# Kernel tuning notes

Measured on AMD Instinct MI355X. Metric: run time of the kernel, lower is better.

The kernel has to match this reference:

```python
import jax, jax.numpy as jnp
import numpy as np

N = 50000      # num nodes
HID = 64       # hidden_dim
N2V = 64       # node2vec dim
E = 800000     # num edges
EP = 100000    # prediction edges
L = 2          # num_layers
EPS = 1e-5     # BatchNorm eps


def setup_inputs() -> dict:
    key = jax.random.key(0)
    ks = jax.random.split(key, 8)
    edge_index = jax.random.randint(ks[0], (2, E), 0, N)
    pred_edge = jax.random.randint(ks[1], (EP, 2), 0, N)
    id_emb = jax.random.normal(ks[2], (N, HID), jnp.float32) * 0.1      # learnable ID embedding
    n2v_emb = jax.random.normal(ks[3], (N, N2V), jnp.float32) * 0.1     # frozen node2vec embedding
    proj_w = jax.random.normal(ks[4], (HID + N2V, HID), jnp.float32) / np.sqrt(HID + N2V)
    proj_b = jnp.zeros((HID,), jnp.float32)
    conv_w = jax.random.normal(ks[5], (L, HID, HID), jnp.float32) / np.sqrt(HID)
    conv_b = jnp.zeros((L, HID), jnp.float32)
    bn_gamma = jnp.ones((L, HID), jnp.float32)
    bn_beta = jnp.zeros((L, HID), jnp.float32)
    return {"edge_index": edge_index, "pred_edge": pred_edge, "id_emb": id_emb,
            "n2v_emb": n2v_emb, "proj_w": proj_w, "proj_b": proj_b,
            "conv_w": conv_w, "conv_b": conv_b, "bn_gamma": bn_gamma, "bn_beta": bn_beta}


def reference(edge_index, pred_edge, id_emb, n2v_emb, proj_w, proj_b, conv_w, conv_b, bn_gamma, bn_beta):
    # input projection of concatenated embeddings: [N, HID+N2V] @ [HID+N2V, HID]
    x = jnp.concatenate([id_emb, n2v_emb], axis=1) @ proj_w + proj_b

    # GCN normalization with self-loops: norm_e = d^-1/2[src] * d^-1/2[dst]
    loops = jnp.arange(N, dtype=edge_index.dtype)
    row = jnp.concatenate([edge_index[0], loops])   # source nodes
    col = jnp.concatenate([edge_index[1], loops])   # destination nodes
    deg = jax.ops.segment_sum(jnp.ones(row.shape, x.dtype), col, num_segments=N)
    dis = jnp.where(deg > 0, jax.lax.rsqrt(deg), 0.0)
    norm = dis[row] * dis[col]                      # [E+N]

    for l in range(L):
        h = x @ conv_w[l]                                                    # [N, HID]
        agg = jax.ops.segment_sum(norm[:, None] * h[row], col, num_segments=N) + conv_b[l]
        # BatchNorm1d (training-mode batch stats over nodes)
        mu = agg.mean(axis=0)
        var = agg.var(axis=0)
        xn = (agg - mu) * jax.lax.rsqrt(var + EPS) * bn_gamma[l] + bn_beta[l]
        x = x + jax.nn.relu(xn)                                              # residual (shapes match)

    # dot-product link decoder
    z = x
    return (z[pred_edge[:, 0]] * z[pred_edge[:, 1]]).sum(axis=1)
```

## Files before the change

### kernel.cpp

```cpp
#include <hip/hip_runtime.h>

#define NN 50000
#define HID 64
#define NE 800000
#define NP 100000
#define BN_EPS 1e-5f
#define NB1 196
#define MAXDEG 96

static inline size_t alignup(size_t x) { return (x + 255) & ~(size_t)255; }

__device__ __forceinline__ void f4fma(float a, const float4& w, float4& c) {
    c.x += a * w.x; c.y += a * w.y; c.z += a * w.z; c.w += a * w.w;
}
__device__ __forceinline__ void f4add(const float4& a, float4& c) {
    c.x += a.x; c.y += a.y; c.z += a.z; c.w += a.w;
}
__device__ __forceinline__ unsigned bfpack(float a, float b) {
    unsigned ua = __float_as_uint(a), ub = __float_as_uint(b);
    ua = (ua + 0x7fffu + ((ua >> 16) & 1u)) >> 16;
    ub = (ub + 0x7fffu + ((ub >> 16) & 1u)) >> 16;
    return ua | (ub << 16);
}
__device__ __forceinline__ float4 bf2f4(uint2 u) {
    float4 r;
    r.x = __uint_as_float(u.x << 16);
    r.y = __uint_as_float(u.x & 0xffff0000u);
    r.z = __uint_as_float(u.y << 16);
    r.w = __uint_as_float(u.y & 0xffff0000u);
    return r;
}


__global__ __launch_bounds__(256) void k_zero(int* __restrict__ cnt, float* __restrict__ sums) {
    int i = blockIdx.x * blockDim.x + threadIdx.x;
    if (i < NN) cnt[i] = 0;
    if (i < 256) sums[i] = 0.f;
}


__global__ __launch_bounds__(256) void k_countfill(const int* __restrict__ row,
                                                   const int* __restrict__ col,
                                                   int* __restrict__ cnt,
                                                   unsigned short* __restrict__ csr) {
    int e = blockIdx.x * blockDim.x + threadIdx.x;
    if (e >= NE) return;
    int d = col[e];
    int r = atomicAdd(&cnt[d], 1);
    csr[d * MAXDEG + r] = (unsigned short)row[e];
}


__global__ __launch_bounds__(256) void k_proj(const float* __restrict__ id_emb,
                                              const float* __restrict__ n2v,
                                              const float* __restrict__ W,
                                              const float* __restrict__ b,
                                              const int* __restrict__ cnt,
                                              float* __restrict__ x,
                                              unsigned short* __restrict__ xh) {
    __shared__ unsigned short Wlh[128 * 64];
    __shared__ unsigned short Al[32 * 132];
    int tid = threadIdx.x;
    int node0 = blockIdx.x * 32;
    const float2* W2f = (const float2*)W;
#pragma unroll
    for (int it = 0; it < 16; ++it) {
        int i = it * 256 + tid;
        float2 w = W2f[i];
        *(unsigned*)&Wlh[2 * i] = bfpack(w.x, w.y);
    }
    const float2* id2 = (const float2*)id_emb;
    const float2* nv2 = (const float2*)n2v;
#pragma unroll
    for (int it = 0; it < 8; ++it) {
        int i = it * 256 + tid;
        int r = i >> 6, kp = i & 63;
        int n = node0 + r;
        float2 v = make_float2(0.f, 0.f);
        if (n < NN) v = (kp < 32) ? id2[n * 32 + kp] : nv2[n * 32 + (kp - 32)];
        *(unsigned*)&Al[r * 132 + 2 * kp] = bfpack(v.x, v.y);
    }
    __syncthreads();
    int sub = tid >> 4, q = tid & 15;
    const uint2* W2 = (const uint2*)Wlh;
    float4* x4 = (float4*)x;
    uint2* xh2 = (uint2*)xh;
    float4 bb = ((const float4*)b)[q];
    float4 c0 = bb, c1 = bb;
#pragma unroll 4
    for (int k4 = 0; k4 < 32; ++k4) {
        float4 w0 = bf2f4(W2[(k4 * 4 + 0) * 16 + q]);
        float4 w1 = bf2f4(W2[(k4 * 4 + 1) * 16 + q]);
        float4 w2 = bf2f4(W2[(k4 * 4 + 2) * 16 + q]);
        float4 w3 = bf2f4(W2[(k4 * 4 + 3) * 16 + q]);
        float4 a0 = bf2f4(*(const uint2*)&Al[(sub * 2 + 0) * 132 + k4 * 4]);
        float4 a1 = bf2f4(*(const uint2*)&Al[(sub * 2 + 1) * 132 + k4 * 4]);
        f4fma(a0.x, w0, c0); f4fma(a0.y, w1, c0); f4fma(a0.z, w2, c0); f4fma(a0.w, w3, c0);
        f4fma(a1.x, w0, c1); f4fma(a1.y, w1, c1); f4fma(a1.z, w2, c1); f4fma(a1.w, w3, c1);
    }
    int n0 = node0 + sub * 2;
    if (n0 + 0 < NN) { float d = rsqrtf((float)(cnt[n0+0] + 1)); x4[(n0+0)*16+q] = c0;
        xh2[(n0+0)*16+q] = make_uint2(bfpack(c0.x*d,c0.y*d), bfpack(c0.z*d,c0.w*d)); }
    if (n0 + 1 < NN) { float d = rsqrtf((float)(cnt[n0+1] + 1)); x4[(n0+1)*16+q] = c1;
        xh2[(n0+1)*16+q] = make_uint2(bfpack(c1.x*d,c1.y*d), bfpack(c1.z*d,c1.w*d)); }
}


__global__ __launch_bounds__(256) void k_gather(const int* __restrict__ cnt,
                                                const unsigned short* __restrict__ csr,
                                                const unsigned short* __restrict__ xh,
                                                unsigned short* __restrict__ th) {
    int gw = (blockIdx.x * blockDim.x + threadIdx.x) >> 6;
    int lane = threadIdx.x & 63;
    int sub = lane >> 4, q = lane & 15;
    int node = gw * 4 + sub;
    if (node >= NN) return;
    const uint2* xh2 = (const uint2*)xh;
    float4 acc = make_float4(0.f, 0.f, 0.f, 0.f);
    const unsigned short* cs = csr + node * MAXDEG;
    int c = cnt[node];
    int jj = 0;
    for (; jj + 7 < c; jj += 8) {
        uint4 s8 = *(const uint4*)(cs + jj);
        int s0 = s8.x & 0xffff, s1 = s8.x >> 16;
        int s2 = s8.y & 0xffff, s3 = s8.y >> 16;
        int s4 = s8.z & 0xffff, s5 = s8.z >> 16;
        int s6 = s8.w & 0xffff, s7 = s8.w >> 16;
        uint2 u0 = xh2[s0 * 16 + q];
        uint2 u1 = xh2[s1 * 16 + q];
        uint2 u2 = xh2[s2 * 16 + q];
        uint2 u3 = xh2[s3 * 16 + q];
        uint2 u4 = xh2[s4 * 16 + q];
        uint2 u5 = xh2[s5 * 16 + q];
        uint2 u6 = xh2[s6 * 16 + q];
        uint2 u7 = xh2[s7 * 16 + q];
        f4add(bf2f4(u0), acc); f4add(bf2f4(u1), acc);
        f4add(bf2f4(u2), acc); f4add(bf2f4(u3), acc);
        f4add(bf2f4(u4), acc); f4add(bf2f4(u5), acc);
        f4add(bf2f4(u6), acc); f4add(bf2f4(u7), acc);
    }
    for (; jj < c; ++jj) {
        uint2 u0 = xh2[cs[jj] * 16 + q];
        f4add(bf2f4(u0), acc);
    }
    f4add(bf2f4(xh2[node * 16 + q]), acc);
    float di = rsqrtf((float)(c + 1));
    acc.x *= di; acc.y *= di; acc.z *= di; acc.w *= di;
    ((uint2*)th)[node * 16 + q] = make_uint2(bfpack(acc.x, acc.y), bfpack(acc.z, acc.w));
}


__global__ __launch_bounds__(256) void k_gemm_stats(const unsigned short* __restrict__ th,
                                                    const float* __restrict__ W,
                                                    unsigned short* __restrict__ agg,
                                                    float* __restrict__ sums) {
    __shared__ float Wl[64 * 64];
    __shared__ float ls0[16][64];
    __shared__ float ls1[16][64];
    int tid = threadIdx.x;
    for (int i = tid; i < 64 * 64; i += 256) Wl[i] = W[i];
    __syncthreads();
    int sub = tid >> 4, q = tid & 15;
    const uint2* t2 = (const uint2*)th;
    const float4* W4 = (const float4*)Wl;
    uint2* agg2 = (uint2*)agg;
    float4 s1 = make_float4(0.f, 0.f, 0.f, 0.f), s2 = s1;
#pragma unroll
    for (int gg = 0; gg < 2; ++gg) {
        int g = blockIdx.x * 2 + gg;
        int n0 = g * 64 + sub * 4;
        int r0 = min(n0 + 0, NN - 1), r1 = min(n0 + 1, NN - 1);
        int r2 = min(n0 + 2, NN - 1), r3 = min(n0 + 3, NN - 1);
        float4 c0 = make_float4(0.f,0.f,0.f,0.f), c1 = c0, c2 = c0, c3 = c0;
#pragma unroll 4
        for (int k4 = 0; k4 < 16; ++k4) {
            float4 a0 = bf2f4(t2[r0 * 16 + k4]);
            float4 a1 = bf2f4(t2[r1 * 16 + k4]);
            float4 a2 = bf2f4(t2[r2 * 16 + k4]);
            float4 a3 = bf2f4(t2[r3 * 16 + k4]);
            float4 w0 = W4[(k4 * 4 + 0) * 16 + q];
            float4 w1 = W4[(k4 * 4 + 1) * 16 + q];
            float4 w2 = W4[(k4 * 4 + 2) * 16 + q];
            float4 w3 = W4[(k4 * 4 + 3) * 16 + q];
            f4fma(a0.x, w0, c0); f4fma(a0.y, w1, c0); f4fma(a0.z, w2, c0); f4fma(a0.w, w3, c0);
            f4fma(a1.x, w0, c1); f4fma(a1.y, w1, c1); f4fma(a1.z, w2, c1); f4fma(a1.w, w3, c1);
            f4fma(a2.x, w0, c2); f4fma(a2.y, w1, c2); f4fma(a2.z, w2, c2); f4fma(a2.w, w3, c2);
            f4fma(a3.x, w0, c3); f4fma(a3.y, w1, c3); f4fma(a3.z, w2, c3); f4fma(a3.w, w3, c3);
        }
        if (n0 + 0 < NN) { agg2[(n0 + 0) * 16 + q] = make_uint2(bfpack(c0.x, c0.y), bfpack(c0.z, c0.w));
            s1.x += c0.x; s1.y += c0.y; s1.z += c0.z; s1.w += c0.w;
            s2.x += c0.x*c0.x; s2.y += c0.y*c0.y; s2.z += c0.z*c0.z; s2.w += c0.w*c0.w; }
        if (n0 + 1 < NN) { agg2[(n0 + 1) * 16 + q] = make_uint2(bfpack(c1.x, c1.y), bfpack(c1.z, c1.w));
            s1.x += c1.x; s1.y += c1.y; s1.z += c1.z; s1.w += c1.w;
            s2.x += c1.x*c1.x; s2.y += c1.y*c1.y; s2.z += c1.z*c1.z; s2.w += c1.w*c1.w; }
        if (n0 + 2 < NN) { agg2[(n0 + 2) * 16 + q] = make_uint2(bfpack(c2.x, c2.y), bfpack(c2.z, c2.w));
            s1.x += c2.x; s1.y += c2.y; s1.z += c2.z; s1.w += c2.w;
            s2.x += c2.x*c2.x; s2.y += c2.y*c2.y; s2.z += c2.z*c2.z; s2.w += c2.w*c2.w; }
        if (n0 + 3 < NN) { agg2[(n0 + 3) * 16 + q] = make_uint2(bfpack(c3.x, c3.y), bfpack(c3.z, c3.w));
            s1.x += c3.x; s1.y += c3.y; s1.z += c3.z; s1.w += c3.w;
            s2.x += c3.x*c3.x; s2.y += c3.y*c3.y; s2.z += c3.z*c3.z; s2.w += c3.w*c3.w; }
    }
    ls0[sub][q * 4 + 0] = s1.x; ls0[sub][q * 4 + 1] = s1.y;
    ls0[sub][q * 4 + 2] = s1.z; ls0[sub][q * 4 + 3] = s1.w;
    ls1[sub][q * 4 + 0] = s2.x; ls1[sub][q * 4 + 1] = s2.y;
    ls1[sub][q * 4 + 2] = s2.z; ls1[sub][q * 4 + 3] = s2.w;
    __syncthreads();
    if (tid < 64) {
        float a = 0.f;
#pragma unroll
        for (int r = 0; r < 16; ++r) a += ls0[r][tid];
        atomicAdd(&sums[tid], a);
    } else if (tid < 128) {
        int c = tid - 64;
        float a = 0.f;
#pragma unroll
        for (int r = 0; r < 16; ++r) a += ls1[r][c];
        atomicAdd(&sums[64 + c], a);
    }
}


__global__ __launch_bounds__(256) void k_bnupdate(const unsigned short* __restrict__ agg,
                                                  const float* __restrict__ sums,
                                                  const float* __restrict__ gamma,
                                                  const float* __restrict__ beta,
                                                  const int* __restrict__ cnt,
                                                  int prescale,
                                                  float* __restrict__ x,
                                                  unsigned short* __restrict__ xh) {
    int i = blockIdx.x * blockDim.x + threadIdx.x;
    if (i >= NN * 16) return;
    int f4 = i & 15;
    const float invn = 1.0f / (float)NN;
    float4 sm = ((const float4*)sums)[f4];
    float4 sq = ((const float4*)(sums + 64))[f4];
    float4 g = ((const float4*)gamma)[f4];
    float4 be = ((const float4*)beta)[f4];
    float4 a = bf2f4(((const uint2*)agg)[i]);
    float4 xv = ((const float4*)x)[i];
    float mu, var, rstd, xn;
    mu = sm.x * invn; var = sq.x * invn - mu * mu; rstd = rsqrtf(var + BN_EPS);
    xn = (a.x - mu) * rstd * g.x + be.x; xv.x += fmaxf(xn, 0.f);
    mu = sm.y * invn; var = sq.y * invn - mu * mu; rstd = rsqrtf(var + BN_EPS);
    xn = (a.y - mu) * rstd * g.y + be.y; xv.y += fmaxf(xn, 0.f);
    mu = sm.z * invn; var = sq.z * invn - mu * mu; rstd = rsqrtf(var + BN_EPS);
    xn = (a.z - mu) * rstd * g.z + be.z; xv.z += fmaxf(xn, 0.f);
    mu = sm.w * invn; var = sq.w * invn - mu * mu; rstd = rsqrtf(var + BN_EPS);
    xn = (a.w - mu) * rstd * g.w + be.w; xv.w += fmaxf(xn, 0.f);
    if (prescale) {
        ((float4*)x)[i] = xv;
        float d = rsqrtf((float)(cnt[i >> 4] + 1));
        ((uint2*)xh)[i] = make_uint2(bfpack(xv.x * d, xv.y * d), bfpack(xv.z * d, xv.w * d));
    } else {
        ((uint2*)xh)[i] = make_uint2(bfpack(xv.x, xv.y), bfpack(xv.z, xv.w));
    }
}


__global__ __launch_bounds__(256) void k_decode(const int* __restrict__ pred,
                                                const unsigned short* __restrict__ zh,
                                                float* __restrict__ out) {
    int gw = (blockIdx.x * blockDim.x + threadIdx.x) >> 6;
    int lane = threadIdx.x & 63;
    int sub = lane >> 4, q = lane & 15;
    int p = gw * 4 + sub;
    if (p >= NP) return;
    const uint2* z2 = (const uint2*)zh;
    int a = pred[2 * p], b = pred[2 * p + 1];
    float4 va = bf2f4(z2[a * 16 + q]);
    float4 vb = bf2f4(z2[b * 16 + q]);
    float v = va.x * vb.x + va.y * vb.y + va.z * vb.z + va.w * vb.w;
    v += __shfl_xor(v, 1);
    v += __shfl_xor(v, 2);
    v += __shfl_xor(v, 4);
    v += __shfl_xor(v, 8);
    if (q == 0) out[p] = v;
}

extern "C" void kernel_launch(void* const* d_in, const int* in_sizes, int n_in,
                              void* d_out, int out_size, void* d_ws, size_t ws_size,
                              hipStream_t stream) {
    const int* edge_index = (const int*)d_in[0];
    const int* pred       = (const int*)d_in[1];
    const float* id_emb   = (const float*)d_in[2];
    const float* n2v      = (const float*)d_in[3];
    const float* proj_w   = (const float*)d_in[4];
    const float* proj_b   = (const float*)d_in[5];
    const float* conv_w   = (const float*)d_in[6];
    const float* gamma    = (const float*)d_in[8];
    const float* beta     = (const float*)d_in[9];
    float* out = (float*)d_out;

    char* ws = (char*)d_ws;
    size_t off = 0;
    int* cnt     = (int*)(ws + off);   off += alignup(NN * 4);
    unsigned short* csr = (unsigned short*)(ws + off); off += alignup((size_t)NN * MAXDEG * 2);
    float* x     = (float*)(ws + off); off += alignup((size_t)NN * 64 * 4);
    unsigned short* agg = (unsigned short*)(ws + off); off += alignup((size_t)NN * 64 * 2);
    unsigned short* xh = (unsigned short*)(ws + off); off += alignup((size_t)NN * 64 * 2);
    unsigned short* th = (unsigned short*)(ws + off); off += alignup((size_t)NN * 64 * 2);
    float* sums  = (float*)(ws + off);

    const int* row = edge_index;
    const int* col = edge_index + NE;

    k_zero<<<NB1, 256, 0, stream>>>(cnt, sums);
    k_countfill<<<(NE + 255) / 256, 256, 0, stream>>>(row, col, cnt, csr);

    k_proj<<<(NN + 31) / 32, 256, 0, stream>>>(id_emb, n2v, proj_w, proj_b, cnt, x, xh);

    for (int l = 0; l < 2; ++l) {
        k_gather<<<((NN + 3) / 4 * 64 + 255) / 256, 256, 0, stream>>>(cnt, csr, xh, th);
        k_gemm_stats<<<391, 256, 0, stream>>>(th, conv_w + l * 64 * 64, agg, sums + l * 128);
        k_bnupdate<<<(NN * 16 + 255) / 256, 256, 0, stream>>>(agg, sums + l * 128, gamma + l * 64,
                                                              beta + l * 64, cnt, (l == 0) ? 1 : 0, x, xh);
    }

    k_decode<<<(NP / 4 * 64 + 255) / 256, 256, 0, stream>>>(pred, xh, out);
}
```

Before: 192.0 us.

## Split edge count/fill and co-schedule with projection in merged kernels

After: 191.3 us. About the same (-0.3%).

```diff
diff --git a/kernel.cpp b/kernel.cpp
--- a/kernel.cpp
+++ b/kernel.cpp
@@ -7,6 +7,9 @@
 #define BN_EPS 1e-5f
 #define NB1 196
 #define MAXDEG 96
+#define NB_EDGE 3125
+#define NB_PROJ 1563
+#define NB_SCALE 3125
 
 static inline size_t alignup(size_t x) { return (x + 255) & ~(size_t)255; }
 
@@ -39,29 +42,23 @@
 }
 
 
-__global__ __launch_bounds__(256) void k_countfill(const int* __restrict__ row,
-                                                   const int* __restrict__ col,
-                                                   int* __restrict__ cnt,
-                                                   unsigned short* __restrict__ csr) {
-    int e = blockIdx.x * blockDim.x + threadIdx.x;
-    if (e >= NE) return;
-    int d = col[e];
-    int r = atomicAdd(&cnt[d], 1);
-    csr[d * MAXDEG + r] = (unsigned short)row[e];
-}
-
-
-__global__ __launch_bounds__(256) void k_proj(const float* __restrict__ id_emb,
-                                              const float* __restrict__ n2v,
-                                              const float* __restrict__ W,
-                                              const float* __restrict__ b,
-                                              const int* __restrict__ cnt,
-                                              float* __restrict__ x,
-                                              unsigned short* __restrict__ xh) {
+__global__ __launch_bounds__(256) void k_count_proj(const int* __restrict__ row,
+                                                    const int* __restrict__ col,
+                                                    int* __restrict__ cnt, int* __restrict__ rank,
+                                                    const float* __restrict__ id_emb,
+                                                    const float* __restrict__ n2v,
+                                                    const float* __restrict__ W,
+                                                    const float* __restrict__ b,
+                                                    float* __restrict__ x) {
     __shared__ unsigned short Wlh[128 * 64];
     __shared__ unsigned short Al[32 * 132];
     int tid = threadIdx.x;
-    int node0 = blockIdx.x * 32;
+    if (blockIdx.x < NB_EDGE) {
+        int e = blockIdx.x * 256 + tid;
+        if (e < NE) rank[e] = atomicAdd(&cnt[col[e]], 1);
+        return;
+    }
+    int node0 = (blockIdx.x - NB_EDGE) * 32;
     const float2* W2f = (const float2*)W;
 #pragma unroll
     for (int it = 0; it < 16; ++it) {
@@ -84,7 +81,6 @@
     int sub = tid >> 4, q = tid & 15;
     const uint2* W2 = (const uint2*)Wlh;
     float4* x4 = (float4*)x;
-    uint2* xh2 = (uint2*)xh;
     float4 bb = ((const float4*)b)[q];
     float4 c0 = bb, c1 = bb;
 #pragma unroll 4
@@ -99,10 +95,29 @@
         f4fma(a1.x, w0, c1); f4fma(a1.y, w1, c1); f4fma(a1.z, w2, c1); f4fma(a1.w, w3, c1);
     }
     int n0 = node0 + sub * 2;
-    if (n0 + 0 < NN) { float d = rsqrtf((float)(cnt[n0+0] + 1)); x4[(n0+0)*16+q] = c0;
-        xh2[(n0+0)*16+q] = make_uint2(bfpack(c0.x*d,c0.y*d), bfpack(c0.z*d,c0.w*d)); }
-    if (n0 + 1 < NN) { float d = rsqrtf((float)(cnt[n0+1] + 1)); x4[(n0+1)*16+q] = c1;
-        xh2[(n0+1)*16+q] = make_uint2(bfpack(c1.x*d,c1.y*d), bfpack(c1.z*d,c1.w*d)); }
+    if (n0 + 0 < NN) x4[(n0 + 0) * 16 + q] = c0;
+    if (n0 + 1 < NN) x4[(n0 + 1) * 16 + q] = c1;
+}
+
+
+__global__ __launch_bounds__(256) void k_fill_scale(const int* __restrict__ row,
+                                                    const int* __restrict__ col,
+                                                    const int* __restrict__ rank,
+                                                    const int* __restrict__ cnt,
+                                                    unsigned short* __restrict__ csr,
+                                                    const float* __restrict__ x,
+                                                    unsigned short* __restrict__ xh) {
+    int tid = threadIdx.x;
+    if (blockIdx.x < NB_EDGE) {
+        int e = blockIdx.x * 256 + tid;
+        if (e < NE) csr[col[e] * MAXDEG + rank[e]] = (unsigned short)row[e];
+        return;
+    }
+    int i = (blockIdx.x - NB_EDGE) * 256 + tid;
+    if (i >= NN * 16) return;
+    float4 xv = ((const float4*)x)[i];
+    float d = rsqrtf((float)(cnt[i >> 4] + 1));
+    ((uint2*)xh)[i] = make_uint2(bfpack(xv.x * d, xv.y * d), bfpack(xv.z * d, xv.w * d));
 }
 
 
@@ -294,6 +309,7 @@
     char* ws = (char*)d_ws;
     size_t off = 0;
     int* cnt     = (int*)(ws + off);   off += alignup(NN * 4);
+    int* rank    = (int*)(ws + off);   off += alignup((size_t)NE * 4);
     unsigned short* csr = (unsigned short*)(ws + off); off += alignup((size_t)NN * MAXDEG * 2);
     float* x     = (float*)(ws + off); off += alignup((size_t)NN * 64 * 4);
     unsigned short* agg = (unsigned short*)(ws + off); off += alignup((size_t)NN * 64 * 2);
@@ -305,9 +321,9 @@
     const int* col = edge_index + NE;
 
     k_zero<<<NB1, 256, 0, stream>>>(cnt, sums);
-    k_countfill<<<(NE + 255) / 256, 256, 0, stream>>>(row, col, cnt, csr);
-
-    k_proj<<<(NN + 31) / 32, 256, 0, stream>>>(id_emb, n2v, proj_w, proj_b, cnt, x, xh);
+    k_count_proj<<<NB_EDGE + NB_PROJ, 256, 0, stream>>>(row, col, cnt, rank,
+                                                        id_emb, n2v, proj_w, proj_b, x);
+    k_fill_scale<<<NB_EDGE + NB_SCALE, 256, 0, stream>>>(row, col, rank, cnt, csr, x, xh);
 
     for (int l = 0; l < 2; ++l) {
         k_gather<<<((NN + 3) / 4 * 64 + 255) / 256, 256, 0, stream>>>(cnt, csr, xh, th);
```
